# Performance work log

Hardware: AMD Instinct MI355X
Metric: run time of the kernel (lower is better)

## Reference

```python
import jax, jax.numpy as jnp
import numpy as np

N = 100000
E = 1600000
HID = 128

def _leaky(x, s=0.01):
    return jax.nn.leaky_relu(x, s)

def gat_conv(x, src, dst, W, a_src, a_dst, bias, heads, out_ch, concat):
    # x: [N, F_in]; W: [F_in, heads*out_ch]; a_src/a_dst: [heads, out_ch]
    n = x.shape[0]
    h = (x @ W).reshape(n, heads, out_ch)                      # [N,H,C]
    al_s = jnp.einsum('nhc,hc->nh', h, a_src)                  # [N,H]
    al_d = jnp.einsum('nhc,hc->nh', h, a_dst)
    e = jax.nn.leaky_relu(al_s[src] + al_d[dst], 0.2)          # [E,H]
    m = jax.ops.segment_max(e, dst, num_segments=n)            # [N,H]
    ex = jnp.exp(e - m[dst])
    den = jax.ops.segment_sum(ex, dst, num_segments=n) + 1e-16
    alpha = ex / den[dst]                                      # [E,H]
    out = jax.ops.segment_sum(alpha[:, :, None] * h[src], dst, num_segments=n)  # [N,H,C]
    out = out.reshape(n, heads * out_ch) if concat else out.mean(axis=1)
    return out + bias

def setup_inputs() -> dict:
    key = jax.random.key(0)
    ks = jax.random.split(key, 32)
    f32 = jnp.float32
    def rn(k, shape, scale=0.02):
        return jax.random.normal(k, shape, dtype=f32) * scale
    inp = {
        'des': jax.random.normal(ks[0], (N, 768), dtype=f32),
        'tweet': jax.random.normal(ks[1], (N, 768), dtype=f32),
        'num_prop': jax.random.normal(ks[2], (N, 5), dtype=f32),
        'cat_prop': jax.random.normal(ks[3], (N, 3), dtype=f32),
        'edge_index': jax.random.randint(ks[4], (2, E), 0, N, dtype=jnp.int64),
        # per-modality encoders -> hidden//4 = 32
        'W_des': rn(ks[5], (768, 32)), 'b_des': jnp.zeros((32,), f32),
        'W_tw': rn(ks[6], (768, 32)), 'b_tw': jnp.zeros((32,), f32),
        'W_np': rn(ks[7], (5, 32)),  'b_np': jnp.zeros((32,), f32),
        'W_cp': rn(ks[8], (3, 32)),  'b_cp': jnp.zeros((32,), f32),
        'W_in': rn(ks[9], (HID, HID)), 'b_in': jnp.zeros((HID,), f32),
        # gat1: in=128, out=32, heads=4, concat -> 128
        'gat1_W': rn(ks[10], (HID, 4 * 32)),
        'gat1_asrc': rn(ks[11], (4, 32), 0.1), 'gat1_adst': rn(ks[12], (4, 32), 0.1),
        'gat1_b': jnp.zeros((HID,), f32),
        # gat2: in=128, out=128, heads=1
        'gat2_W': rn(ks[13], (HID, HID)),
        'gat2_asrc': rn(ks[14], (1, HID), 0.1), 'gat2_adst': rn(ks[15], (1, HID), 0.1),
        'gat2_b': jnp.zeros((HID,), f32),
        'W_o1': rn(ks[16], (HID, HID)), 'b_o1': jnp.zeros((HID,), f32),
        'W_o2': rn(ks[17], (HID, 2)),  'b_o2': jnp.zeros((2,), f32),
    }
    return inp

def reference(des, tweet, num_prop, cat_prop, edge_index,
              W_des, b_des, W_tw, b_tw, W_np, b_np, W_cp, b_cp,
              W_in, b_in, gat1_W, gat1_asrc, gat1_adst, gat1_b,
              gat2_W, gat2_asrc, gat2_adst, gat2_b,
              W_o1, b_o1, W_o2, b_o2):
    n = des.shape[0]
    # add self loops (PyG GATConv default)
    loop = jnp.arange(n, dtype=edge_index.dtype)
    src = jnp.concatenate([edge_index[0], loop])
    dst = jnp.concatenate([edge_index[1], loop])
    d = _leaky(des @ W_des + b_des)
    t = _leaky(tweet @ W_tw + b_tw)
    np_ = _leaky(num_prop @ W_np + b_np)
    c = _leaky(cat_prop @ W_cp + b_cp)
    x = jnp.concatenate([d, t, np_, c], axis=1)            # [N,128]
    x = _leaky(x @ W_in + b_in)
    x = gat_conv(x, src, dst, gat1_W, gat1_asrc, gat1_adst, gat1_b, 4, 32, True)
    # dropout is identity in eval mode
    x = gat_conv(x, src, dst, gat2_W, gat2_asrc, gat2_adst, gat2_b, 1, HID, True)
    x = _leaky(x @ W_o1 + b_o1)
    return x @ W_o2 + b_o2
```

## Files before the change

### kernel.cpp

```cpp
#include <hip/hip_runtime.h>
#include <cstdint>
#include <cstddef>


typedef __bf16 bf16x8 __attribute__((ext_vector_type(8)));
typedef float f32x4 __attribute__((ext_vector_type(4)));
typedef unsigned short u16x4 __attribute__((ext_vector_type(4)));

static __device__ __forceinline__ float bf2f(unsigned short u){
    unsigned int x = ((unsigned int)u) << 16;
    return __builtin_bit_cast(float, x);
}
static __device__ __forceinline__ unsigned short f2bf(float f){
    unsigned int u = __builtin_bit_cast(unsigned int, f);
    unsigned int r = u + 0x7fffu + ((u >> 16) & 1u);
    return (unsigned short)(r >> 16);
}
static __device__ __forceinline__ void splitf(float v, unsigned short& h, unsigned short& l){
    h = f2bf(v);
    l = f2bf(v - bf2f(h));
}
static __device__ __forceinline__ float leaky01(float v){ return v > 0.f ? v : 0.01f * v; }
static __device__ __forceinline__ float leaky02(float v){ return v > 0.f ? v : 0.2f  * v; }

__global__ void k_detect(const int* __restrict__ ei32, int* __restrict__ eflag){
    int t = threadIdx.x;
    int v = ei32[2*t + 1];
    unsigned long long nz = __ballot(v != 0);
    if (t == 0) eflag[0] = (nz == 0ull) ? 2 : 1;
}

__global__ __launch_bounds__(256) void k_prep_enc(
    const float* __restrict__ Wd, const float* __restrict__ Wtw,
    unsigned short* __restrict__ encW)
{
    int idx = blockIdx.x * 256 + threadIdx.x;
    if (idx >= 2*24576) return;
    int mod = idx / 24576, r = idx % 24576;
    int c = r / 768, k = r % 768;
    const float* W = mod ? Wtw : Wd;
    unsigned short h, l; splitf(W[(size_t)k*32 + c], h, l);
    encW[(size_t)mod*49152 + c*768 + k]         = h;
    encW[(size_t)mod*49152 + 24576 + c*768 + k] = l;
}
__global__ __launch_bounds__(256) void k_prep_mid(
    const float* __restrict__ W0, const float* __restrict__ W1,
    const float* __restrict__ W2, const float* __restrict__ W3,
    unsigned short* __restrict__ midW)
{
    int idx = blockIdx.x * 256 + threadIdx.x;
    if (idx >= 4*16384) return;
    int m = idx / 16384, r = idx % 16384;
    int k = r >> 7, c = r & 127;
    const float* W = m == 0 ? W0 : m == 1 ? W1 : m == 2 ? W2 : W3;
    unsigned short h, l; splitf(W[(size_t)k*128 + c], h, l);
    int g = (k >> 3) ^ (c & 15);
    size_t base = (size_t)m * 32768;
    midW[base + c*128 + g*8 + (k & 7)]         = h;
    midW[base + 16384 + c*128 + g*8 + (k & 7)] = l;
}

__global__ __launch_bounds__(256) void k_enc(
    const float* __restrict__ des, const float* __restrict__ bd,
    const float* __restrict__ twt, const float* __restrict__ bt,
    const unsigned short* __restrict__ encW,
    float* __restrict__ x0, int n)
{
    const float* A; const float* bias; int colofs; const unsigned short* Wb;
    if (blockIdx.y == 0){ A = des; bias = bd; colofs = 0;  Wb = encW; }
    else                { A = twt; bias = bt; colofs = 32; Wb = encW + 49152; }

    int lane = threadIdx.x & 63, wave = threadIdx.x >> 6;
    int rowBase = blockIdx.x * 64 + wave * 16;
    int arow = rowBase + (lane & 15); if (arow >= n) arow = n - 1;
    int kg = (lane >> 4) * 8;
    const float* Ap = A + (size_t)arow * 768 + kg;
    const unsigned short* W0p = Wb + (lane & 15) * 768 + kg;
    const unsigned short* W1p = Wb + (16 + (lane & 15)) * 768 + kg;

    f32x4 acc0 = {0.f,0.f,0.f,0.f}, acc1 = {0.f,0.f,0.f,0.f};
    #pragma unroll 4
    for (int k0 = 0; k0 < 768; k0 += 32){
        f32x4 a0 = *(const f32x4*)(Ap + k0);
        f32x4 a1 = *(const f32x4*)(Ap + k0 + 4);
        bf16x8 ah, al;
        #pragma unroll
        for (int i = 0; i < 4; ++i){
            unsigned short h, l; splitf(a0[i], h, l);
            ah[i] = __builtin_bit_cast(__bf16, h);
            al[i] = __builtin_bit_cast(__bf16, l);
        }
        #pragma unroll
        for (int i = 0; i < 4; ++i){
            unsigned short h, l; splitf(a1[i], h, l);
            ah[4+i] = __builtin_bit_cast(__bf16, h);
            al[4+i] = __builtin_bit_cast(__bf16, l);
        }
        bf16x8 b0h = *(const bf16x8*)(W0p + k0);
        bf16x8 b0l = *(const bf16x8*)(W0p + 24576 + k0);
        bf16x8 b1h = *(const bf16x8*)(W1p + k0);
        bf16x8 b1l = *(const bf16x8*)(W1p + 24576 + k0);
        acc0 = __builtin_amdgcn_mfma_f32_16x16x32_bf16(ah, b0h, acc0, 0, 0, 0);
        acc0 = __builtin_amdgcn_mfma_f32_16x16x32_bf16(al, b0h, acc0, 0, 0, 0);
        acc0 = __builtin_amdgcn_mfma_f32_16x16x32_bf16(ah, b0l, acc0, 0, 0, 0);
        acc1 = __builtin_amdgcn_mfma_f32_16x16x32_bf16(ah, b1h, acc1, 0, 0, 0);
        acc1 = __builtin_amdgcn_mfma_f32_16x16x32_bf16(al, b1h, acc1, 0, 0, 0);
        acc1 = __builtin_amdgcn_mfma_f32_16x16x32_bf16(ah, b1l, acc1, 0, 0, 0);
    }

    float bc0 = bias[lane & 15];
    float bc1 = bias[16 + (lane & 15)];
    int r0 = rowBase + ((lane >> 4) << 2);
    #pragma unroll
    for (int r = 0; r < 4; ++r){
        int rr = r0 + r;
        if (rr < n){
            x0[(size_t)rr*128 + colofs + (lane & 15)]      = leaky01(acc0[r] + bc0);
            x0[(size_t)rr*128 + colofs + 16 + (lane & 15)] = leaky01(acc1[r] + bc1);
        }
    }
}

__global__ __launch_bounds__(256) void k_npcp(
    const float* __restrict__ npv, const float* __restrict__ Wnp,
    const float* __restrict__ bnp,
    const float* __restrict__ cpv, const float* __restrict__ Wcp,
    const float* __restrict__ bcp,
    float* __restrict__ x0, int n)
{
    __shared__ float w5[160], w3[96], bb[64];
    int tid = threadIdx.x;
    if (tid < 160) w5[tid] = Wnp[tid];
    if (tid >= 160 && tid < 256) w3[tid - 160] = Wcp[tid - 160];
    if (tid < 32) bb[tid] = bnp[tid];
    if (tid >= 32 && tid < 64) bb[tid] = bcp[tid - 32];
    __syncthreads();

    int node = blockIdx.x * 256 + tid;
    if (node >= n) return;
    float a[5], b3[3];
    #pragma unroll
    for (int i = 0; i < 5; ++i) a[i] = npv[(size_t)node*5 + i];
    #pragma unroll
    for (int i = 0; i < 3; ++i) b3[i] = cpv[(size_t)node*3 + i];
    float* xo = x0 + (size_t)node * 128;
    #pragma unroll
    for (int c = 0; c < 32; c += 4){
        f32x4 o1, o2;
        #pragma unroll
        for (int u = 0; u < 4; ++u){
            float s = bb[c + u];
            #pragma unroll
            for (int i = 0; i < 5; ++i) s += a[i] * w5[i*32 + c + u];
            o1[u] = leaky01(s);
            float t = bb[32 + c + u];
            #pragma unroll
            for (int i = 0; i < 3; ++i) t += b3[i] * w3[i*32 + c + u];
            o2[u] = leaky01(t);
        }
        *(f32x4*)(xo + 64 + c) = o1;
        *(f32x4*)(xo + 96 + c) = o2;
    }
}

__global__ __launch_bounds__(256) void k_mid(
    const float* __restrict__ A, const unsigned short* __restrict__ midWm,
    const float* __restrict__ bias, float* __restrict__ C, int n, int act)
{
    __shared__ unsigned short Ah[64*128];
    __shared__ unsigned short Al[64*128];
    int tid = threadIdx.x;
    int rowBase = blockIdx.x * 64;
    for (int q = tid; q < 64*32; q += 256){
        int r = q >> 5, c4 = (q & 31) * 4;
        int gr = rowBase + r; if (gr >= n) gr = n - 1;
        f32x4 v = *(const f32x4*)(A + (size_t)gr*128 + c4);
        unsigned short hh[4], ll[4];
        #pragma unroll
        for (int i = 0; i < 4; ++i) splitf(v[i], hh[i], ll[i]);
        int g = (c4 >> 3) ^ (r & 15);
        int off = r*128 + g*8 + (c4 & 7);
        u16x4 th = {hh[0], hh[1], hh[2], hh[3]};
        u16x4 tl = {ll[0], ll[1], ll[2], ll[3]};
        *(u16x4*)(&Ah[off]) = th;
        *(u16x4*)(&Al[off]) = tl;
    }
    __syncthreads();

    int lane = tid & 63, wave = tid >> 6;
    int mr = lane & 15;
    int kg = (lane >> 4) * 8;
    int wrow = wave * 16 + mr;
    f32x4 acc[8];
    #pragma unroll
    for (int i = 0; i < 8; ++i) acc[i] = (f32x4){0.f,0.f,0.f,0.f};

    #pragma unroll
    for (int k0 = 0; k0 < 128; k0 += 32){
        int gidx = (k0 + kg) >> 3;
        int aoff = wrow*128 + ((gidx ^ mr) * 8);
        bf16x8 ahf = *(const bf16x8*)(&Ah[aoff]);
        bf16x8 alf = *(const bf16x8*)(&Al[aoff]);
        #pragma unroll
        for (int ct = 0; ct < 8; ++ct){
            int brow = ct*16 + mr;
            int woff = brow*128 + ((gidx ^ mr) * 8);
            bf16x8 bh = *(const bf16x8*)(midWm + woff);
            bf16x8 bl = *(const bf16x8*)(midWm + 16384 + woff);
            acc[ct] = __builtin_amdgcn_mfma_f32_16x16x32_bf16(ahf, bh, acc[ct], 0, 0, 0);
            acc[ct] = __builtin_amdgcn_mfma_f32_16x16x32_bf16(alf, bh, acc[ct], 0, 0, 0);
            acc[ct] = __builtin_amdgcn_mfma_f32_16x16x32_bf16(ahf, bl, acc[ct], 0, 0, 0);
        }
    }

    int r0 = rowBase + wave*16 + ((lane >> 4) << 2);
    #pragma unroll
    for (int ct = 0; ct < 8; ++ct){
        int cc = ct*16 + mr;
        float bv = act ? bias[cc] : 0.f;
        #pragma unroll
        for (int r = 0; r < 4; ++r){
            int rr = r0 + r;
            if (rr < n){
                float v = acc[ct][r] + bv;
                if (act) v = leaky01(v);
                C[(size_t)rr*128 + cc] = v;
            }
        }
    }
}

__global__ __launch_bounds__(256) void k_al(
    const float* __restrict__ h, const float* __restrict__ a_src,
    const float* __restrict__ a_dst, float* __restrict__ als,
    float* __restrict__ ald, int n, int heads)
{
    int lane = threadIdx.x & 63, wave = threadIdx.x >> 6;
    int node = blockIdx.x * 4 + wave;
    if (node >= n) return;
    float2 hv = *(const float2*)(h + (size_t)node*128 + lane*2);
    float2 asv = *(const float2*)(a_src + lane*2);
    float2 adv = *(const float2*)(a_dst + lane*2);
    float ps = hv.x*asv.x + hv.y*asv.y;
    float pd = hv.x*adv.x + hv.y*adv.y;
    #pragma unroll
    for (int ofs = 1; ofs <= 8; ofs <<= 1){
        ps += __shfl_xor(ps, ofs);
        pd += __shfl_xor(pd, ofs);
    }
    if (heads == 1){
        ps += __shfl_xor(ps, 16); pd += __shfl_xor(pd, 16);
        ps += __shfl_xor(ps, 32); pd += __shfl_xor(pd, 32);
        if (lane == 0){ als[node] = ps; ald[node] = pd; }
    } else {
        if ((lane & 15) == 0){
            als[(size_t)node*4 + (lane >> 4)] = ps;
            ald[(size_t)node*4 + (lane >> 4)] = pd;
        }
    }
}

__global__ __launch_bounds__(256) void k_edge4(
    const float* __restrict__ h, const float* __restrict__ als, const float* __restrict__ ald,
    const int* __restrict__ startv, const int* __restrict__ degv, const int* __restrict__ col,
    const float* __restrict__ bias, float* __restrict__ outp, int n)
{
    int lane = threadIdx.x & 63, wave = threadIdx.x >> 6;
    int node = blockIdx.x * 4 + wave;
    if (node >= n) return;
    int hl = lane >> 4;
    int st = startv[node], dg = degv[node];
    f32x4 sAls = *(const f32x4*)(als + (size_t)node*4);
    f32x4 sAld = *(const f32x4*)(ald + (size_t)node*4);
    float es[4], m[4];
    #pragma unroll
    for (int t = 0; t < 4; ++t){ es[t] = leaky02(sAls[t] + sAld[t]); m[t] = es[t]; }

    int mycol = 0; f32x4 myals = {0.f,0.f,0.f,0.f};
    bool have = lane < dg;
    if (have){
        mycol = col[st + lane];
        myals = *(const f32x4*)(als + (size_t)mycol*4);
    }
    float e4[4];
    #pragma unroll
    for (int t = 0; t < 4; ++t){
        e4[t] = have ? leaky02(myals[t] + sAld[t]) : -3.0e38f;
        m[t] = fmaxf(m[t], e4[t]);
    }
    #pragma unroll
    for (int ofs = 1; ofs <= 32; ofs <<= 1){
        #pragma unroll
        for (int t = 0; t < 4; ++t) m[t] = fmaxf(m[t], __shfl_xor(m[t], ofs));
    }
    float w4[4];
    #pragma unroll
    for (int t = 0; t < 4; ++t) w4[t] = have ? __expf(e4[t] - m[t]) : 0.f;

    float wself = __expf(es[hl] - m[hl]);
    float den = wself;
    float2 hs = *(const float2*)(h + (size_t)node*128 + lane*2);
    float acc0 = wself * hs.x, acc1 = wself * hs.y;

    int nin = dg < 64 ? dg : 64;
    for (int j = 0; j < nin; ++j){
        int s = __shfl(mycol, j);
        float wv0 = __shfl(w4[0], j), wv1 = __shfl(w4[1], j);
        float wv2 = __shfl(w4[2], j), wv3 = __shfl(w4[3], j);
        float wgt = hl == 0 ? wv0 : hl == 1 ? wv1 : hl == 2 ? wv2 : wv3;
        float2 hv = *(const float2*)(h + (size_t)s*128 + lane*2);
        den += wgt;
        acc0 += wgt * hv.x; acc1 += wgt * hv.y;
    }
    for (int j = 64; j < dg; ++j){
        int s = col[st + j];
        float asv = als[(size_t)s*4 + hl];
        float wgt = __expf(leaky02(asv + sAld[hl]) - m[hl]);
        float2 hv = *(const float2*)(h + (size_t)s*128 + lane*2);
        den += wgt; acc0 += wgt * hv.x; acc1 += wgt * hv.y;
    }
    float inv = 1.0f / (den + 1e-16f);
    float2 bv = *(const float2*)(bias + lane*2);
    float2 o; o.x = acc0 * inv + bv.x; o.y = acc1 * inv + bv.y;
    *(float2*)(outp + (size_t)node*128 + lane*2) = o;
}

__global__ __launch_bounds__(256) void k_edge1(
    const float* __restrict__ h, const float* __restrict__ als, const float* __restrict__ ald,
    const int* __restrict__ startv, const int* __restrict__ degv, const int* __restrict__ col,
    const float* __restrict__ bias, float* __restrict__ outp, int n)
{
    int lane = threadIdx.x & 63, wave = threadIdx.x >> 6;
    int node = blockIdx.x * 4 + wave;
    if (node >= n) return;
    int st = startv[node], dg = degv[node];
    float sa = als[node], sd = ald[node];
    float es = leaky02(sa + sd);
    float m = es;
    int mycol = 0; float myals = 0.f;
    bool have = lane < dg;
    if (have){ mycol = col[st + lane]; myals = als[mycol]; }
    float e1 = have ? leaky02(myals + sd) : -3.0e38f;
    m = fmaxf(m, e1);
    #pragma unroll
    for (int ofs = 1; ofs <= 32; ofs <<= 1) m = fmaxf(m, __shfl_xor(m, ofs));
    float w1 = have ? __expf(e1 - m) : 0.f;

    float wself = __expf(es - m);
    float den = wself;
    float2 hs = *(const float2*)(h + (size_t)node*128 + lane*2);
    float acc0 = wself * hs.x, acc1 = wself * hs.y;

    int nin = dg < 64 ? dg : 64;
    for (int j = 0; j < nin; ++j){
        int s = __shfl(mycol, j);
        float wgt = __shfl(w1, j);
        float2 hv = *(const float2*)(h + (size_t)s*128 + lane*2);
        den += wgt; acc0 += wgt * hv.x; acc1 += wgt * hv.y;
    }
    for (int j = 64; j < dg; ++j){
        int s = col[st + j];
        float wgt = __expf(leaky02(als[s] + sd) - m);
        float2 hv = *(const float2*)(h + (size_t)s*128 + lane*2);
        den += wgt; acc0 += wgt * hv.x; acc1 += wgt * hv.y;
    }
    float inv = 1.0f / (den + 1e-16f);
    float2 bv = *(const float2*)(bias + lane*2);
    float2 o; o.x = acc0 * inv + bv.x; o.y = acc1 * inv + bv.y;
    *(float2*)(outp + (size_t)node*128 + lane*2) = o;
}

__global__ __launch_bounds__(256) void k_out(
    const float* __restrict__ x3, const float* __restrict__ Wo2,
    const float* __restrict__ bo2, float* __restrict__ outp, int n)
{
    int lane = threadIdx.x & 63, wave = threadIdx.x >> 6;
    int node = blockIdx.x * 4 + wave;
    if (node >= n) return;
    float xa = x3[(size_t)node*128 + lane];
    float xb = x3[(size_t)node*128 + 64 + lane];
    float s0 = xa * Wo2[lane*2]     + xb * Wo2[(lane + 64)*2];
    float s1 = xa * Wo2[lane*2 + 1] + xb * Wo2[(lane + 64)*2 + 1];
    #pragma unroll
    for (int ofs = 1; ofs <= 32; ofs <<= 1){
        s0 += __shfl_xor(s0, ofs);
        s1 += __shfl_xor(s1, ofs);
    }
    if (lane == 0){
        outp[(size_t)node*2]     = s0 + bo2[0];
        outp[(size_t)node*2 + 1] = s1 + bo2[1];
    }
}

__global__ void k_hist(const int* __restrict__ ei32, const int* __restrict__ eflag,
                       int* __restrict__ deg, int e){
    int st = eflag[0];
    int i = blockIdx.x * 256 + threadIdx.x;
    if (i < e) atomicAdd(&deg[ei32[(size_t)st*(e + i)]], 1);
}
__global__ __launch_bounds__(256) void k_scan1(
    const int* __restrict__ deg, int* __restrict__ startv, int* __restrict__ bsum, int n)
{
    __shared__ int sd[256];
    int tid = threadIdx.x;
    int base = blockIdx.x * 2048 + tid * 8;
    int v[8]; int s = 0;
    #pragma unroll
    for (int i = 0; i < 8; ++i){
        int x = (base + i < n) ? deg[base + i] : 0;
        v[i] = s; s += x;
    }
    sd[tid] = s; __syncthreads();
    int own = s;
    for (int ofs = 1; ofs < 256; ofs <<= 1){
        int t = 0; if (tid >= ofs) t = sd[tid - ofs];
        __syncthreads(); sd[tid] += t; __syncthreads();
    }
    int excl = sd[tid] - own;
    #pragma unroll
    for (int i = 0; i < 8; ++i)
        if (base + i < n) startv[base + i] = excl + v[i];
    if (tid == 255) bsum[blockIdx.x] = sd[255];
}
__global__ void k_scan2(const int* __restrict__ bsum, int* __restrict__ bofs, int nb){
    if (threadIdx.x == 0 && blockIdx.x == 0){
        int run = 0;
        for (int i = 0; i < nb; ++i){ bofs[i] = run; run += bsum[i]; }
    }
}
__global__ void k_scan3(const int* __restrict__ bofs, int* __restrict__ startv,
                        int* __restrict__ cursor, int n){
    int i = blockIdx.x * 256 + threadIdx.x;
    if (i < n){
        int v = startv[i] + bofs[i >> 11];
        startv[i] = v; cursor[i] = v;
    }
}
__global__ void k_scatter(const int* __restrict__ ei32, const int* __restrict__ eflag,
                          int* __restrict__ cursor, int* __restrict__ col, int e){
    int st = eflag[0];
    int i = blockIdx.x * 256 + threadIdx.x;
    if (i < e){
        int s = ei32[(size_t)st*i];
        int d = ei32[(size_t)st*(e + i)];
        int pos = atomicAdd(&cursor[d], 1);
        col[pos] = s;
    }
}

extern "C" void kernel_launch(void* const* d_in, const int* in_sizes, int n_in,
                              void* d_out, int out_size, void* d_ws, size_t ws_size,
                              hipStream_t stream)
{
    const int n = in_sizes[0] / 768;
    const int e = in_sizes[4] / 2;

    const float* des  = (const float*)d_in[0];
    const float* twt  = (const float*)d_in[1];
    const float* npv  = (const float*)d_in[2];
    const float* cpv  = (const float*)d_in[3];
    const int*   ei   = (const int*)d_in[4];
    const float* W_des = (const float*)d_in[5];
    const float* b_des = (const float*)d_in[6];
    const float* W_tw  = (const float*)d_in[7];
    const float* b_tw  = (const float*)d_in[8];
    const float* W_np  = (const float*)d_in[9];
    const float* b_np  = (const float*)d_in[10];
    const float* W_cp  = (const float*)d_in[11];
    const float* b_cp  = (const float*)d_in[12];
    const float* W_in  = (const float*)d_in[13];
    const float* b_in  = (const float*)d_in[14];
    const float* g1W   = (const float*)d_in[15];
    const float* g1as  = (const float*)d_in[16];
    const float* g1ad  = (const float*)d_in[17];
    const float* g1b   = (const float*)d_in[18];
    const float* g2W   = (const float*)d_in[19];
    const float* g2as  = (const float*)d_in[20];
    const float* g2ad  = (const float*)d_in[21];
    const float* g2b   = (const float*)d_in[22];
    const float* Wo1   = (const float*)d_in[23];
    const float* bo1   = (const float*)d_in[24];
    const float* Wo2   = (const float*)d_in[25];
    const float* bo2   = (const float*)d_in[26];

    char* wp = (char*)d_ws;
    size_t off = 0;
    auto alloc = [&](size_t bytes) -> void* {
        void* p = (void*)(wp + off);
        off += (bytes + 255) & ~(size_t)255;
        return p;
    };
    int*            eflag = (int*)alloc(256);
    unsigned short* encW  = (unsigned short*)alloc((size_t)2*49152*2);
    unsigned short* midW  = (unsigned short*)alloc((size_t)4*32768*2);
    float* buf0   = (float*)alloc((size_t)n * 128 * 4);
    float* buf1   = (float*)alloc((size_t)n * 128 * 4);
    float* als1   = (float*)alloc((size_t)n * 4 * 4);
    float* ald1   = (float*)alloc((size_t)n * 4 * 4);
    float* als2   = (float*)alloc((size_t)n * 4);
    float* ald2   = (float*)alloc((size_t)n * 4);
    int*   deg    = (int*)alloc((size_t)n * 4);
    int*   startv = (int*)alloc((size_t)n * 4);
    int*   cursor = (int*)alloc((size_t)n * 4);
    int*   col    = (int*)alloc((size_t)e * 4);
    int*   bsum   = (int*)alloc(256 * 4);
    int*   bofs   = (int*)alloc(256 * 4);

    k_detect<<<1, 64, 0, stream>>>(ei, eflag);
    k_prep_enc<<<(2*24576 + 255)/256, 256, 0, stream>>>(W_des, W_tw, encW);
    k_prep_mid<<<(4*16384 + 255)/256, 256, 0, stream>>>(W_in, g1W, g2W, Wo1, midW);

    hipMemsetAsync(deg, 0, (size_t)n * sizeof(int), stream);
    k_hist<<<(e + 255)/256, 256, 0, stream>>>(ei, eflag, deg, e);
    int nch = (n + 2047) / 2048;
    k_scan1<<<nch, 256, 0, stream>>>(deg, startv, bsum, n);
    k_scan2<<<1, 64, 0, stream>>>(bsum, bofs, nch);
    k_scan3<<<(n + 255)/256, 256, 0, stream>>>(bofs, startv, cursor, n);
    k_scatter<<<(e + 255)/256, 256, 0, stream>>>(ei, eflag, cursor, col, e);

    dim3 ge((n + 63)/64, 2);
    k_enc<<<ge, 256, 0, stream>>>(des, b_des, twt, b_tw, encW, buf0, n);
    k_npcp<<<(n + 255)/256, 256, 0, stream>>>(npv, W_np, b_np, cpv, W_cp, b_cp, buf0, n);

    k_mid<<<(n + 63)/64, 256, 0, stream>>>(buf0, midW,             b_in, buf1, n, 1);
    k_mid<<<(n + 63)/64, 256, 0, stream>>>(buf1, midW + 32768,     b_in, buf0, n, 0);
    k_al<<<(n + 3)/4, 256, 0, stream>>>(buf0, g1as, g1ad, als1, ald1, n, 4);
    k_edge4<<<(n + 3)/4, 256, 0, stream>>>(buf0, als1, ald1, startv, deg, col, g1b, buf1, n);
    k_mid<<<(n + 63)/64, 256, 0, stream>>>(buf1, midW + 2*32768,   b_in, buf0, n, 0);
    k_al<<<(n + 3)/4, 256, 0, stream>>>(buf0, g2as, g2ad, als2, ald2, n, 1);
    k_edge1<<<(n + 3)/4, 256, 0, stream>>>(buf0, als2, ald2, startv, deg, col, g2b, buf1, n);
    k_mid<<<(n + 63)/64, 256, 0, stream>>>(buf1, midW + 3*32768,   bo1, buf0, n, 1);
    k_out<<<(n + 3)/4, 256, 0, stream>>>(buf0, Wo2, bo2, (float*)d_out, n);
}
```

Measured before the change: 1.470 ms.

## Double-buffer encoder A tiles into LDS via async global_load_lds

The des/tweet encoder GEMM now stages 64x64 fp32 A tiles into XOR-swizzled shared memory with direct global-to-LDS loads, double-buffered so the next K-slice loads while MFMAs run on the current one. This is meant to hide the latency of streaming the large 768-wide input rows, which dominate memory traffic. It adds 32KB of LDS per block and a launch_bounds occupancy hint. Each wave reads only its own rows, so there is no block barrier, only a vmcnt wait. Other edits just rename loop variables.

```diff
diff --git a/kernel.cpp b/kernel.cpp
--- a/kernel.cpp
+++ b/kernel.cpp
@@ -22,6 +22,12 @@
 }
 static __device__ __forceinline__ float leaky01(float v){ return v > 0.f ? v : 0.01f * v; }
 static __device__ __forceinline__ float leaky02(float v){ return v > 0.f ? v : 0.2f  * v; }
+
+static __device__ __forceinline__ void gload16(const float* g, const void* l){
+    __builtin_amdgcn_global_load_lds(
+        (const __attribute__((address_space(1))) void*)g,
+        (__attribute__((address_space(3))) void*)l, 16, 0, 0);
+}
 
 __global__ void k_detect(const int* __restrict__ ei32, int* __restrict__ eflag){
     int t = threadIdx.x;
@@ -60,63 +66,104 @@
     midW[base + 16384 + c*128 + g*8 + (k & 7)] = l;
 }
 
-__global__ __launch_bounds__(256) void k_enc(
+__global__ __launch_bounds__(256, 4) void k_enc(
     const float* __restrict__ des, const float* __restrict__ bd,
     const float* __restrict__ twt, const float* __restrict__ bt,
     const unsigned short* __restrict__ encW,
     float* __restrict__ x0, int n)
 {
+    __shared__ float As[2][64*64];
+
     const float* A; const float* bias; int colofs; const unsigned short* Wb;
     if (blockIdx.y == 0){ A = des; bias = bd; colofs = 0;  Wb = encW; }
     else                { A = twt; bias = bt; colofs = 32; Wb = encW + 49152; }
 
     int lane = threadIdx.x & 63, wave = threadIdx.x >> 6;
-    int rowBase = blockIdx.x * 64 + wave * 16;
-    int arow = rowBase + (lane & 15); if (arow >= n) arow = n - 1;
-    int kg = (lane >> 4) * 8;
-    const float* Ap = A + (size_t)arow * 768 + kg;
-    const unsigned short* W0p = Wb + (lane & 15) * 768 + kg;
-    const unsigned short* W1p = Wb + (16 + (lane & 15)) * 768 + kg;
+    int rowBase = blockIdx.x * 64;
+
+    const float* ap0; const float* ap1; const float* ap2; const float* ap3;
+    {
+        const float* tmp[4];
+        #pragma unroll
+        for (int inst = 0; inst < 4; ++inst){
+            int row = wave*16 + inst*4 + (lane >> 4);
+            int gr = rowBase + row; if (gr >= n) gr = n - 1;
+            int lc = (lane & 15) ^ (inst*4 + (lane >> 4));
+            tmp[inst] = A + (size_t)gr*768 + lc*4;
+        }
+        ap0 = tmp[0]; ap1 = tmp[1]; ap2 = tmp[2]; ap3 = tmp[3];
+    }
+
+    int mr = lane & 15;
+    int j  = lane >> 4;
+    const unsigned short* W0p = Wb + mr*768 + j*8;
+    const unsigned short* W1p = Wb + (16 + mr)*768 + j*8;
 
     f32x4 acc0 = {0.f,0.f,0.f,0.f}, acc1 = {0.f,0.f,0.f,0.f};
-    #pragma unroll 4
-    for (int k0 = 0; k0 < 768; k0 += 32){
-        f32x4 a0 = *(const f32x4*)(Ap + k0);
-        f32x4 a1 = *(const f32x4*)(Ap + k0 + 4);
-        bf16x8 ah, al;
-        #pragma unroll
-        for (int i = 0; i < 4; ++i){
-            unsigned short h, l; splitf(a0[i], h, l);
-            ah[i] = __builtin_bit_cast(__bf16, h);
-            al[i] = __builtin_bit_cast(__bf16, l);
-        }
-        #pragma unroll
-        for (int i = 0; i < 4; ++i){
-            unsigned short h, l; splitf(a1[i], h, l);
-            ah[4+i] = __builtin_bit_cast(__bf16, h);
-            al[4+i] = __builtin_bit_cast(__bf16, l);
-        }
-        bf16x8 b0h = *(const bf16x8*)(W0p + k0);
-        bf16x8 b0l = *(const bf16x8*)(W0p + 24576 + k0);
-        bf16x8 b1h = *(const bf16x8*)(W1p + k0);
-        bf16x8 b1l = *(const bf16x8*)(W1p + 24576 + k0);
-        acc0 = __builtin_amdgcn_mfma_f32_16x16x32_bf16(ah, b0h, acc0, 0, 0, 0);
-        acc0 = __builtin_amdgcn_mfma_f32_16x16x32_bf16(al, b0h, acc0, 0, 0, 0);
-        acc0 = __builtin_amdgcn_mfma_f32_16x16x32_bf16(ah, b0l, acc0, 0, 0, 0);
-        acc1 = __builtin_amdgcn_mfma_f32_16x16x32_bf16(ah, b1h, acc1, 0, 0, 0);
-        acc1 = __builtin_amdgcn_mfma_f32_16x16x32_bf16(al, b1h, acc1, 0, 0, 0);
-        acc1 = __builtin_amdgcn_mfma_f32_16x16x32_bf16(ah, b1l, acc1, 0, 0, 0);
-    }
-
-    float bc0 = bias[lane & 15];
-    float bc1 = bias[16 + (lane & 15)];
-    int r0 = rowBase + ((lane >> 4) << 2);
-    #pragma unroll
-    for (int r = 0; r < 4; ++r){
-        int rr = r0 + r;
+    int r = wave*16 + mr;
+
+    {
+        char* lb = (char*)(&As[0][0]) + wave*4096;
+        gload16(ap0,       lb);
+        gload16(ap1,       lb + 1024);
+        gload16(ap2,       lb + 2048);
+        gload16(ap3,       lb + 3072);
+    }
+
+    for (int t = 0; t < 12; ++t){
+        asm volatile("s_waitcnt vmcnt(0)" ::: "memory");
+        __builtin_amdgcn_sched_barrier(0);
+        if (t < 11){
+            int k1 = (t + 1) * 64;
+            char* lb = (char*)(&As[(t + 1) & 1][0]) + wave*4096;
+            gload16(ap0 + k1, lb);
+            gload16(ap1 + k1, lb + 1024);
+            gload16(ap2 + k1, lb + 2048);
+            gload16(ap3 + k1, lb + 3072);
+        }
+        const float* Ab = &As[t & 1][0] + r*64;
+        int k0 = t * 64;
+        #pragma unroll
+        for (int half = 0; half < 2; ++half){
+            int lc0 = half*8 + 2*j;
+            f32x4 a0 = *(const f32x4*)(Ab + ((lc0       ^ mr) * 4));
+            f32x4 a1 = *(const f32x4*)(Ab + (((lc0 + 1) ^ mr) * 4));
+            bf16x8 ah, al;
+            #pragma unroll
+            for (int i = 0; i < 4; ++i){
+                unsigned short h, l; splitf(a0[i], h, l);
+                ah[i] = __builtin_bit_cast(__bf16, h);
+                al[i] = __builtin_bit_cast(__bf16, l);
+            }
+            #pragma unroll
+            for (int i = 0; i < 4; ++i){
+                unsigned short h, l; splitf(a1[i], h, l);
+                ah[4+i] = __builtin_bit_cast(__bf16, h);
+                al[4+i] = __builtin_bit_cast(__bf16, l);
+            }
+            int kk = k0 + half*32;
+            bf16x8 b0h = *(const bf16x8*)(W0p + kk);
+            bf16x8 b0l = *(const bf16x8*)(W0p + 24576 + kk);
+            bf16x8 b1h = *(const bf16x8*)(W1p + kk);
+            bf16x8 b1l = *(const bf16x8*)(W1p + 24576 + kk);
+            acc0 = __builtin_amdgcn_mfma_f32_16x16x32_bf16(ah, b0h, acc0, 0, 0, 0);
+            acc0 = __builtin_amdgcn_mfma_f32_16x16x32_bf16(al, b0h, acc0, 0, 0, 0);
+            acc0 = __builtin_amdgcn_mfma_f32_16x16x32_bf16(ah, b0l, acc0, 0, 0, 0);
+            acc1 = __builtin_amdgcn_mfma_f32_16x16x32_bf16(ah, b1h, acc1, 0, 0, 0);
+            acc1 = __builtin_amdgcn_mfma_f32_16x16x32_bf16(al, b1h, acc1, 0, 0, 0);
+            acc1 = __builtin_amdgcn_mfma_f32_16x16x32_bf16(ah, b1l, acc1, 0, 0, 0);
+        }
+    }
+
+    float bc0 = bias[mr];
+    float bc1 = bias[16 + mr];
+    int r0 = rowBase + wave*16 + (j << 2);
+    #pragma unroll
+    for (int rr4 = 0; rr4 < 4; ++rr4){
+        int rr = r0 + rr4;
         if (rr < n){
-            x0[(size_t)rr*128 + colofs + (lane & 15)]      = leaky01(acc0[r] + bc0);
-            x0[(size_t)rr*128 + colofs + 16 + (lane & 15)] = leaky01(acc1[r] + bc1);
+            x0[(size_t)rr*128 + colofs + mr]      = leaky01(acc0[rr4] + bc0);
+            x0[(size_t)rr*128 + colofs + 16 + mr] = leaky01(acc1[rr4] + bc1);
         }
     }
 }
@@ -219,10 +266,10 @@
         int cc = ct*16 + mr;
         float bv = act ? bias[cc] : 0.f;
         #pragma unroll
-        for (int r = 0; r < 4; ++r){
-            int rr = r0 + r;
+        for (int rr4 = 0; rr4 < 4; ++rr4){
+            int rr = r0 + rr4;
             if (rr < n){
-                float v = acc[ct][r] + bv;
+                float v = acc[ct][rr4] + bv;
                 if (act) v = leaky01(v);
                 C[(size_t)rr*128 + cc] = v;
             }
@@ -303,17 +350,17 @@
     float acc0 = wself * hs.x, acc1 = wself * hs.y;
 
     int nin = dg < 64 ? dg : 64;
-    for (int j = 0; j < nin; ++j){
-        int s = __shfl(mycol, j);
-        float wv0 = __shfl(w4[0], j), wv1 = __shfl(w4[1], j);
-        float wv2 = __shfl(w4[2], j), wv3 = __shfl(w4[3], j);
+    for (int jj = 0; jj < nin; ++jj){
+        int s = __shfl(mycol, jj);
+        float wv0 = __shfl(w4[0], jj), wv1 = __shfl(w4[1], jj);
+        float wv2 = __shfl(w4[2], jj), wv3 = __shfl(w4[3], jj);
         float wgt = hl == 0 ? wv0 : hl == 1 ? wv1 : hl == 2 ? wv2 : wv3;
         float2 hv = *(const float2*)(h + (size_t)s*128 + lane*2);
         den += wgt;
         acc0 += wgt * hv.x; acc1 += wgt * hv.y;
     }
-    for (int j = 64; j < dg; ++j){
-        int s = col[st + j];
+    for (int jj = 64; jj < dg; ++jj){
+        int s = col[st + jj];
         float asv = als[(size_t)s*4 + hl];
         float wgt = __expf(leaky02(asv + sAld[hl]) - m[hl]);
         float2 hv = *(const float2*)(h + (size_t)s*128 + lane*2);
@@ -352,14 +399,14 @@
     float acc0 = wself * hs.x, acc1 = wself * hs.y;
 
     int nin = dg < 64 ? dg : 64;
-    for (int j = 0; j < nin; ++j){
-        int s = __shfl(mycol, j);
-        float wgt = __shfl(w1, j);
+    for (int jj = 0; jj < nin; ++jj){
+        int s = __shfl(mycol, jj);
+        float wgt = __shfl(w1, jj);
         float2 hv = *(const float2*)(h + (size_t)s*128 + lane*2);
         den += wgt; acc0 += wgt * hv.x; acc1 += wgt * hv.y;
     }
-    for (int j = 64; j < dg; ++j){
-        int s = col[st + j];
+    for (int jj = 64; jj < dg; ++jj){
+        int s = col[st + jj];
         float wgt = __expf(leaky02(als[s] + sd) - m);
         float2 hv = *(const float2*)(h + (size_t)s*128 + lane*2);
         den += wgt; acc0 += wgt * hv.x; acc1 += wgt * hv.y;
```

New measurement: 1.425 ms. 1.03x faster.
